# Kernel tuning notes

Hardware: AMD Instinct MI355X
Metric: run time of the kernel (lower is better)

## Reference

```python
import jax, jax.numpy as jnp
import numpy as np

E, N, D = 640000, 10000, 128  # edges, nodes, feature dim (edge=node=global=128)
H, O = 256, 128               # MLP hidden / output dims; concat dim = 4*D = 512


def setup_inputs() -> dict:
    key = jax.random.key(0)
    ks = jax.random.split(key, 7)
    return {
        "edge_attr": jax.random.normal(ks[0], (E, D), dtype=jnp.float32),
        "node_attr": jax.random.normal(ks[1], (N, D), dtype=jnp.float32),
        "global_attr": jax.random.normal(ks[2], (D,), dtype=jnp.float32),
        "senders": jax.random.randint(ks[3], (E,), 0, N),
        "receivers": jax.random.randint(ks[4], (E,), 0, N),
        "W1": jax.random.normal(ks[5], (4 * D, H), dtype=jnp.float32) / np.float32(np.sqrt(4 * D)),
        "b1": jnp.zeros((H,), dtype=jnp.float32),
        "W2": jax.random.normal(ks[6], (H, O), dtype=jnp.float32) / np.float32(np.sqrt(H)),
        "b2": jnp.zeros((O,), dtype=jnp.float32),
    }


def reference(edge_attr, node_attr, global_attr, senders, receivers, W1, b1, W2, b2):
    # Batched form of the per-edge Python loop:
    #   cat([e.data, e.receiver.data, e.sender.data, G.global_attribute.data]) -> updater MLP
    num_edges = edge_attr.shape[0]
    g = jnp.broadcast_to(global_attr, (num_edges, global_attr.shape[0]))  # [E, Dg]
    x = jnp.concatenate(
        [edge_attr, node_attr[receivers], node_attr[senders], g], axis=-1
    )  # [E, 4D]
    h = jax.nn.relu(x @ W1 + b1)  # [E, H]
    return h @ W2 + b2            # [E, O] : updated edge attributes
```

## Files before the change

### kernel.cpp

```cpp
#include <hip/hip_runtime.h>
#include <hip/hip_bf16.h>


typedef __attribute__((ext_vector_type(8))) short bf16x8;
typedef __attribute__((ext_vector_type(4))) float f32x4;
typedef __attribute__((ext_vector_type(2))) unsigned int u32x2;

static __device__ __forceinline__ unsigned short f2bf(float f) {
    unsigned u = __builtin_bit_cast(unsigned, f);
    u += 0x7FFFu + ((u >> 16) & 1u);
    return (unsigned short)(u >> 16);
}

static __device__ __forceinline__ unsigned cvt_pk_bf16(float lo, float hi) {
    unsigned r;
    asm("v_cvt_pk_bf16_f32 %0, %1, %2" : "=v"(r) : "v"(lo), "v"(hi));
    return r;
}


__global__ void prep_node_kernel(const float* __restrict__ node,
                                 ushort* __restrict__ nb) {
    int i = blockIdx.x * 256 + threadIdx.x;
    if (i >= 160000) return;
    const float4* s = (const float4*)(node + (size_t)i * 8);
    float4 a = s[0], b = s[1];
    ushort tmp[8] = { f2bf(a.x), f2bf(a.y), f2bf(a.z), f2bf(a.w),
                      f2bf(b.x), f2bf(b.y), f2bf(b.z), f2bf(b.w) };
    *(bf16x8*)&nb[(size_t)i * 8] = *(bf16x8*)tmp;
}

__global__ void prep_w1_kernel(const float* __restrict__ W1,
                               ushort* __restrict__ w1f) {
    int id = blockIdx.x * 256 + threadIdx.x;
    if (id >= 16 * 12 * 64) return;
    int l = id & 63, blk = id >> 6;
    int ks = blk % 12, gnt = blk / 12;
    int n  = gnt * 16 + (l & 15);
    int k0 = ks * 32 + (l >> 4) * 8;
    ushort tmp[8];
    #pragma unroll
    for (int j = 0; j < 8; ++j) tmp[j] = f2bf(W1[(k0 + j) * 256 + n]);
    *(bf16x8*)&w1f[(size_t)id * 8] = *(bf16x8*)tmp;
}

__global__ void prep_w2_kernel(const float* __restrict__ W2,
                               ushort* __restrict__ w2f) {
    int id = blockIdx.x * 256 + threadIdx.x;
    if (id >= 8 * 8 * 64) return;
    int l = id & 63, blk = id >> 6;
    int ks = blk % 8, gnt = blk / 8;
    int n  = gnt * 16 + (l & 15);
    int k0 = ks * 32 + (l >> 4) * 8;
    ushort tmp[8];
    #pragma unroll
    for (int j = 0; j < 8; ++j) tmp[j] = f2bf(W2[(k0 + j) * 128 + n]);
    *(bf16x8*)&w2f[(size_t)id * 8] = *(bf16x8*)tmp;
}

__global__ void prep_hbias_kernel(const float* __restrict__ W1,
                                  const float* __restrict__ b1,
                                  const float* __restrict__ g,
                                  float* __restrict__ hbias) {
    int n = threadIdx.x;
    float acc = b1[n];
    for (int k = 0; k < 128; ++k) acc += g[k] * W1[(384 + k) * 256 + n];
    hbias[n] = acc;
}


__global__ __launch_bounds__(256, 4) void edge_mlp_kernel(
    const float* __restrict__ edge_attr,
    const int* __restrict__ senders,
    const int* __restrict__ receivers,
    const ushort* __restrict__ node_bf,
    const ushort* __restrict__ w1f,
    const ushort* __restrict__ w2f,
    const float* __restrict__ hbias,
    const float* __restrict__ b2,
    float* __restrict__ out)
{
    __shared__ ushort Lds[64 * 256];
    ushort* Xe = Lds;
    ushort* Hs = Lds;

    const int t    = threadIdx.x;
    const int l    = t & 63;
    const int wid  = t >> 6;
    const int base = blockIdx.x * 64;

    const int lr = l & 15;
    const int q  = l >> 4;
    const int lk = q * 8;

    int nrow[4], srow[4];
    #pragma unroll
    for (int mt = 0; mt < 4; ++mt) {
        int e = base + mt * 16 + lr;
        nrow[mt] = receivers[e] * 128;
        srow[mt] = senders[e]   * 128;
    }

    #pragma unroll
    for (int p = 0; p < 4; ++p) {
        int chunk = p * 256 + t;
        int r  = chunk >> 4;
        int c0 = (chunk & 15) * 8;
        const float4* src = (const float4*)(edge_attr + (size_t)(base + r) * 128 + c0);
        float4 a = src[0];
        float4 b = src[1];
        uint4 uu = { cvt_pk_bf16(a.x, a.y), cvt_pk_bf16(a.z, a.w),
                     cvt_pk_bf16(b.x, b.y), cvt_pk_bf16(b.z, b.w) };
        *(bf16x8*)&Xe[r * 128 + (c0 ^ ((r & 7) << 3))] = __builtin_bit_cast(bf16x8, uu);
    }

    __syncthreads();

    f32x4 acc[4][4];
    #pragma unroll
    for (int mt = 0; mt < 4; ++mt)
        #pragma unroll
        for (int nt = 0; nt < 4; ++nt)
            acc[mt][nt] = (f32x4){0.f, 0.f, 0.f, 0.f};

    #pragma unroll
    for (int ks = 0; ks < 4; ++ks) {
        bf16x8 B[4];
        #pragma unroll
        for (int nt = 0; nt < 4; ++nt)
            B[nt] = *(const bf16x8*)&w1f[(size_t)(((wid * 4 + nt) * 12 + ks) * 64 + l) * 8];
        bf16x8 X[4];
        const int kk = ks * 32 + lk;
        #pragma unroll
        for (int mt = 0; mt < 4; ++mt) {
            const int row = mt * 16 + lr;
            X[mt] = *(const bf16x8*)&Xe[row * 128 + (kk ^ ((row & 7) << 3))];
        }
        #pragma unroll
        for (int mt = 0; mt < 4; ++mt)
            #pragma unroll
            for (int nt = 0; nt < 4; ++nt)
                acc[mt][nt] = __builtin_amdgcn_mfma_f32_16x16x32_bf16(
                    B[nt], X[mt], acc[mt][nt], 0, 0, 0);
    }

    __syncthreads();

    #pragma unroll
    for (int ks = 4; ks < 12; ++ks) {
        bf16x8 B[4];
        #pragma unroll
        for (int nt = 0; nt < 4; ++nt)
            B[nt] = *(const bf16x8*)&w1f[(size_t)(((wid * 4 + nt) * 12 + ks) * 64 + l) * 8];
        const int off = ((ks - 4) & 3) * 32 + lk;
        bf16x8 X[4];
        #pragma unroll
        for (int mt = 0; mt < 4; ++mt)
            X[mt] = *(const bf16x8*)&node_bf[(ks < 8 ? nrow[mt] : srow[mt]) + off];
        #pragma unroll
        for (int mt = 0; mt < 4; ++mt)
            #pragma unroll
            for (int nt = 0; nt < 4; ++nt)
                acc[mt][nt] = __builtin_amdgcn_mfma_f32_16x16x32_bf16(
                    B[nt], X[mt], acc[mt][nt], 0, 0, 0);
    }

    #pragma unroll
    for (int nt = 0; nt < 4; ++nt) {
        const int F = wid * 64 + nt * 16 + q * 4;
        float4 hb4 = *(const float4*)&hbias[F];
        #pragma unroll
        for (int mt = 0; mt < 4; ++mt) {
            float v0 = fmaxf(acc[mt][nt][0] + hb4.x, 0.f);
            float v1 = fmaxf(acc[mt][nt][1] + hb4.y, 0.f);
            float v2 = fmaxf(acc[mt][nt][2] + hb4.z, 0.f);
            float v3 = fmaxf(acc[mt][nt][3] + hb4.w, 0.f);
            u32x2 w = { cvt_pk_bf16(v0, v1), cvt_pk_bf16(v2, v3) };
            const int edge = mt * 16 + lr;
            *(u32x2*)&Hs[edge * 256 + (F ^ ((edge & 7) << 3))] = w;
        }
    }

    __syncthreads();

    f32x4 acc2[4][2];
    #pragma unroll
    for (int mt = 0; mt < 4; ++mt)
        #pragma unroll
        for (int nt = 0; nt < 2; ++nt)
            acc2[mt][nt] = (f32x4){0.f, 0.f, 0.f, 0.f};

    #pragma unroll
    for (int ks = 0; ks < 8; ++ks) {
        bf16x8 W[2];
        #pragma unroll
        for (int nt = 0; nt < 2; ++nt)
            W[nt] = *(const bf16x8*)&w2f[(size_t)(((wid * 2 + nt) * 8 + ks) * 64 + l) * 8];
        bf16x8 Hfr[4];
        const int F = ks * 32 + lk;
        #pragma unroll
        for (int mt = 0; mt < 4; ++mt) {
            const int edge = mt * 16 + lr;
            Hfr[mt] = *(const bf16x8*)&Hs[edge * 256 + (F ^ ((edge & 7) << 3))];
        }
        #pragma unroll
        for (int mt = 0; mt < 4; ++mt)
            #pragma unroll
            for (int nt = 0; nt < 2; ++nt)
                acc2[mt][nt] = __builtin_amdgcn_mfma_f32_16x16x32_bf16(
                    W[nt], Hfr[mt], acc2[mt][nt], 0, 0, 0);
    }

    #pragma unroll
    for (int nt = 0; nt < 2; ++nt) {
        const int F = wid * 32 + nt * 16 + q * 4;
        float4 b24 = *(const float4*)&b2[F];
        #pragma unroll
        for (int mt = 0; mt < 4; ++mt) {
            float4 o = { acc2[mt][nt][0] + b24.x, acc2[mt][nt][1] + b24.y,
                         acc2[mt][nt][2] + b24.z, acc2[mt][nt][3] + b24.w };
            *(float4*)&out[(size_t)(base + mt * 16 + lr) * 128 + F] = o;
        }
    }
}


extern "C" void kernel_launch(void* const* d_in, const int* in_sizes, int n_in,
                              void* d_out, int out_size, void* d_ws, size_t ws_size,
                              hipStream_t stream) {
    (void)in_sizes; (void)n_in; (void)out_size; (void)ws_size;

    const float* edge_attr   = (const float*)d_in[0];
    const float* node_attr   = (const float*)d_in[1];
    const float* global_attr = (const float*)d_in[2];
    const int*   senders     = (const int*)d_in[3];
    const int*   receivers   = (const int*)d_in[4];
    const float* W1          = (const float*)d_in[5];
    const float* b1          = (const float*)d_in[6];
    const float* W2          = (const float*)d_in[7];
    const float* b2          = (const float*)d_in[8];
    float* out = (float*)d_out;

    ushort* node_bf = (ushort*)d_ws;
    ushort* w1f     = (ushort*)((char*)d_ws + 2560000);
    ushort* w2f     = (ushort*)((char*)d_ws + 2756608);
    float*  hbias   = (float*)((char*)d_ws + 2822144);

    hipLaunchKernelGGL(prep_node_kernel,  dim3(625), dim3(256), 0, stream, node_attr, node_bf);
    hipLaunchKernelGGL(prep_w1_kernel,    dim3(48),  dim3(256), 0, stream, W1, w1f);
    hipLaunchKernelGGL(prep_w2_kernel,    dim3(16),  dim3(256), 0, stream, W2, w2f);
    hipLaunchKernelGGL(prep_hbias_kernel, dim3(1),   dim3(256), 0, stream, W1, b1, global_attr, hbias);

    hipLaunchKernelGGL(edge_mlp_kernel, dim3(10000), dim3(256), 0, stream,
                       edge_attr, senders, receivers, node_bf, w1f, w2f, hbias, b2, out);
}
```

Measured before the change: 377.6 us.

## Use 128-edge blocks with 8 waves and double-buffer weight fragment loads

Each block now has 512 threads and handles 128 edges, with two wave rows of 64 edges each sharing the same weight columns. The two layer-1 loops are merged into one 12-step loop. W1 and W2 fragments are prefetched one k-step ahead into double buffers so the global loads overlap the MFMAs. LDS doubles to 64KB per block and register pressure rises from the prefetch buffers, which may lower occupancy.

```diff
diff --git a/kernel.cpp b/kernel.cpp
--- a/kernel.cpp
+++ b/kernel.cpp
@@ -69,7 +69,7 @@
 }
 
 
-__global__ __launch_bounds__(256, 4) void edge_mlp_kernel(
+__global__ __launch_bounds__(512, 4) void edge_mlp_kernel(
     const float* __restrict__ edge_attr,
     const int* __restrict__ senders,
     const int* __restrict__ receivers,
@@ -80,14 +80,16 @@
     const float* __restrict__ b2,
     float* __restrict__ out)
 {
-    __shared__ ushort Lds[64 * 256];
+    __shared__ ushort Lds[128 * 256];
     ushort* Xe = Lds;
     ushort* Hs = Lds;
 
     const int t    = threadIdx.x;
     const int l    = t & 63;
     const int wid  = t >> 6;
-    const int base = blockIdx.x * 64;
+    const int wm   = wid >> 2;
+    const int wn   = wid & 3;
+    const int base = blockIdx.x * 128;
 
     const int lr = l & 15;
     const int q  = l >> 4;
@@ -96,14 +98,14 @@
     int nrow[4], srow[4];
     #pragma unroll
     for (int mt = 0; mt < 4; ++mt) {
-        int e = base + mt * 16 + lr;
+        int e = base + wm * 64 + mt * 16 + lr;
         nrow[mt] = receivers[e] * 128;
         srow[mt] = senders[e]   * 128;
     }
 
     #pragma unroll
     for (int p = 0; p < 4; ++p) {
-        int chunk = p * 256 + t;
+        int chunk = p * 512 + t;
         int r  = chunk >> 4;
         int c0 = (chunk & 15) * 8;
         const float4* src = (const float4*)(edge_attr + (size_t)(base + r) * 128 + c0);
@@ -123,51 +125,47 @@
         for (int nt = 0; nt < 4; ++nt)
             acc[mt][nt] = (f32x4){0.f, 0.f, 0.f, 0.f};
 
-    #pragma unroll
-    for (int ks = 0; ks < 4; ++ks) {
-        bf16x8 B[4];
-        #pragma unroll
-        for (int nt = 0; nt < 4; ++nt)
-            B[nt] = *(const bf16x8*)&w1f[(size_t)(((wid * 4 + nt) * 12 + ks) * 64 + l) * 8];
+    bf16x8 B[2][4];
+    #pragma unroll
+    for (int nt = 0; nt < 4; ++nt)
+        B[0][nt] = *(const bf16x8*)&w1f[(size_t)(((wn * 4 + nt) * 12 + 0) * 64 + l) * 8];
+
+    #pragma unroll
+    for (int ks = 0; ks < 12; ++ks) {
+        const int cur = ks & 1;
+        if (ks < 11) {
+            #pragma unroll
+            for (int nt = 0; nt < 4; ++nt)
+                B[cur ^ 1][nt] = *(const bf16x8*)&w1f[
+                    (size_t)(((wn * 4 + nt) * 12 + (ks + 1)) * 64 + l) * 8];
+        }
         bf16x8 X[4];
-        const int kk = ks * 32 + lk;
-        #pragma unroll
-        for (int mt = 0; mt < 4; ++mt) {
-            const int row = mt * 16 + lr;
-            X[mt] = *(const bf16x8*)&Xe[row * 128 + (kk ^ ((row & 7) << 3))];
+        if (ks < 4) {
+            const int kk = ks * 32 + lk;
+            #pragma unroll
+            for (int mt = 0; mt < 4; ++mt) {
+                const int row = wm * 64 + mt * 16 + lr;
+                X[mt] = *(const bf16x8*)&Xe[row * 128 + (kk ^ ((row & 7) << 3))];
+            }
+        } else {
+            const int off = (ks & 3) * 32 + lk;
+            #pragma unroll
+            for (int mt = 0; mt < 4; ++mt)
+                X[mt] = *(const bf16x8*)&node_bf[(ks < 8 ? nrow[mt] : srow[mt]) + off];
         }
         #pragma unroll
         for (int mt = 0; mt < 4; ++mt)
             #pragma unroll
             for (int nt = 0; nt < 4; ++nt)
                 acc[mt][nt] = __builtin_amdgcn_mfma_f32_16x16x32_bf16(
-                    B[nt], X[mt], acc[mt][nt], 0, 0, 0);
+                    B[cur][nt], X[mt], acc[mt][nt], 0, 0, 0);
     }
 
     __syncthreads();
 
     #pragma unroll
-    for (int ks = 4; ks < 12; ++ks) {
-        bf16x8 B[4];
-        #pragma unroll
-        for (int nt = 0; nt < 4; ++nt)
-            B[nt] = *(const bf16x8*)&w1f[(size_t)(((wid * 4 + nt) * 12 + ks) * 64 + l) * 8];
-        const int off = ((ks - 4) & 3) * 32 + lk;
-        bf16x8 X[4];
-        #pragma unroll
-        for (int mt = 0; mt < 4; ++mt)
-            X[mt] = *(const bf16x8*)&node_bf[(ks < 8 ? nrow[mt] : srow[mt]) + off];
-        #pragma unroll
-        for (int mt = 0; mt < 4; ++mt)
-            #pragma unroll
-            for (int nt = 0; nt < 4; ++nt)
-                acc[mt][nt] = __builtin_amdgcn_mfma_f32_16x16x32_bf16(
-                    B[nt], X[mt], acc[mt][nt], 0, 0, 0);
-    }
-
-    #pragma unroll
     for (int nt = 0; nt < 4; ++nt) {
-        const int F = wid * 64 + nt * 16 + q * 4;
+        const int F = wn * 64 + nt * 16 + q * 4;
         float4 hb4 = *(const float4*)&hbias[F];
         #pragma unroll
         for (int mt = 0; mt < 4; ++mt) {
@@ -176,7 +174,7 @@
             float v2 = fmaxf(acc[mt][nt][2] + hb4.z, 0.f);
             float v3 = fmaxf(acc[mt][nt][3] + hb4.w, 0.f);
             u32x2 w = { cvt_pk_bf16(v0, v1), cvt_pk_bf16(v2, v3) };
-            const int edge = mt * 16 + lr;
+            const int edge = wm * 64 + mt * 16 + lr;
             *(u32x2*)&Hs[edge * 256 + (F ^ ((edge & 7) << 3))] = w;
         }
     }
@@ -190,17 +188,25 @@
         for (int nt = 0; nt < 2; ++nt)
             acc2[mt][nt] = (f32x4){0.f, 0.f, 0.f, 0.f};
 
+    bf16x8 W2b[2][2];
+    #pragma unroll
+    for (int nt = 0; nt < 2; ++nt)
+        W2b[0][nt] = *(const bf16x8*)&w2f[(size_t)(((wn * 2 + nt) * 8 + 0) * 64 + l) * 8];
+
     #pragma unroll
     for (int ks = 0; ks < 8; ++ks) {
-        bf16x8 W[2];
-        #pragma unroll
-        for (int nt = 0; nt < 2; ++nt)
-            W[nt] = *(const bf16x8*)&w2f[(size_t)(((wid * 2 + nt) * 8 + ks) * 64 + l) * 8];
+        const int cur = ks & 1;
+        if (ks < 7) {
+            #pragma unroll
+            for (int nt = 0; nt < 2; ++nt)
+                W2b[cur ^ 1][nt] = *(const bf16x8*)&w2f[
+                    (size_t)(((wn * 2 + nt) * 8 + (ks + 1)) * 64 + l) * 8];
+        }
         bf16x8 Hfr[4];
         const int F = ks * 32 + lk;
         #pragma unroll
         for (int mt = 0; mt < 4; ++mt) {
-            const int edge = mt * 16 + lr;
+            const int edge = wm * 64 + mt * 16 + lr;
             Hfr[mt] = *(const bf16x8*)&Hs[edge * 256 + (F ^ ((edge & 7) << 3))];
         }
         #pragma unroll
@@ -208,18 +214,18 @@
             #pragma unroll
             for (int nt = 0; nt < 2; ++nt)
                 acc2[mt][nt] = __builtin_amdgcn_mfma_f32_16x16x32_bf16(
-                    W[nt], Hfr[mt], acc2[mt][nt], 0, 0, 0);
+                    W2b[cur][nt], Hfr[mt], acc2[mt][nt], 0, 0, 0);
     }
 
     #pragma unroll
     for (int nt = 0; nt < 2; ++nt) {
-        const int F = wid * 32 + nt * 16 + q * 4;
+        const int F = wn * 32 + nt * 16 + q * 4;
         float4 b24 = *(const float4*)&b2[F];
         #pragma unroll
         for (int mt = 0; mt < 4; ++mt) {
             float4 o = { acc2[mt][nt][0] + b24.x, acc2[mt][nt][1] + b24.y,
                          acc2[mt][nt][2] + b24.z, acc2[mt][nt][3] + b24.w };
-            *(float4*)&out[(size_t)(base + mt * 16 + lr) * 128 + F] = o;
+            *(float4*)&out[(size_t)(base + wm * 64 + mt * 16 + lr) * 128 + F] = o;
         }
     }
 }
@@ -251,6 +257,6 @@
     hipLaunchKernelGGL(prep_w2_kernel,    dim3(16),  dim3(256), 0, stream, W2, w2f);
     hipLaunchKernelGGL(prep_hbias_kernel, dim3(1),   dim3(256), 0, stream, W1, b1, global_attr, hbias);
 
-    hipLaunchKernelGGL(edge_mlp_kernel, dim3(10000), dim3(256), 0, stream,
+    hipLaunchKernelGGL(edge_mlp_kernel, dim3(5000), dim3(512), 0, stream,
                        edge_attr, senders, receivers, node_bf, w1f, w2f, hbias, b2, out);
 }
```

New measurement: 427.2 us. +13.2%, slower.

## Precompute per-node W1 projections and gather them instead of node features

Applied to the files above, without the earlier changes.

Splits the first layer algebraically: each node's receiver and sender contributions (node_attr @ W1 slices, plus the global bias folded into the receiver part) are computed once per node in a new prep kernel and stored as bf16. The edge kernel then only runs the edge-feature K=128 GEMM and adds the two gathered 256-wide projections before ReLU. This cuts the layer-1 MFMA work per edge by two thirds, but gathers twice as many bytes per node and adds an extra bf16 rounding of the projections. It also double-buffers the weight fragment loads, separates the Xe and Hs LDS buffers, and lowers the occupancy hint from 4 to 3.

```diff
diff --git a/kernel.cpp b/kernel.cpp
--- a/kernel.cpp
+++ b/kernel.cpp
@@ -18,17 +18,13 @@
     return r;
 }
 
-
-__global__ void prep_node_kernel(const float* __restrict__ node,
-                                 ushort* __restrict__ nb) {
-    int i = blockIdx.x * 256 + threadIdx.x;
-    if (i >= 160000) return;
-    const float4* s = (const float4*)(node + (size_t)i * 8);
-    float4 a = s[0], b = s[1];
-    ushort tmp[8] = { f2bf(a.x), f2bf(a.y), f2bf(a.z), f2bf(a.w),
-                      f2bf(b.x), f2bf(b.y), f2bf(b.z), f2bf(b.w) };
-    *(bf16x8*)&nb[(size_t)i * 8] = *(bf16x8*)tmp;
-}
+static __device__ __forceinline__ float bflo(unsigned u) {
+    return __builtin_bit_cast(float, u << 16);
+}
+static __device__ __forceinline__ float bfhi(unsigned u) {
+    return __builtin_bit_cast(float, u & 0xFFFF0000u);
+}
+
 
 __global__ void prep_w1_kernel(const float* __restrict__ W1,
                                ushort* __restrict__ w1f) {
@@ -68,21 +64,100 @@
     hbias[n] = acc;
 }
 
-
-__global__ __launch_bounds__(256, 4) void edge_mlp_kernel(
+__global__ __launch_bounds__(256) void prep_proj_kernel(
+    const float* __restrict__ node_attr,
+    const ushort* __restrict__ w1f,
+    const float* __restrict__ hbias,
+    ushort* __restrict__ Pr,
+    ushort* __restrict__ Ps)
+{
+    __shared__ ushort Xn[64 * 128];
+
+    const int t = threadIdx.x, l = t & 63, wn = t >> 6;
+    const int base = blockIdx.x * 64;
+    const int lr = l & 15, q = l >> 4, lk = q * 8;
+
+    #pragma unroll
+    for (int p = 0; p < 4; ++p) {
+        int chunk = p * 256 + t;
+        int r  = chunk >> 4;
+        int c0 = (chunk & 15) * 8;
+        int node = base + r; if (node >= 10000) node = 9999;
+        const float4* src = (const float4*)(node_attr + (size_t)node * 128 + c0);
+        float4 a = src[0];
+        float4 b = src[1];
+        uint4 uu = { cvt_pk_bf16(a.x, a.y), cvt_pk_bf16(a.z, a.w),
+                     cvt_pk_bf16(b.x, b.y), cvt_pk_bf16(b.z, b.w) };
+        *(bf16x8*)&Xn[r * 128 + (c0 ^ ((r & 7) << 3))] = __builtin_bit_cast(bf16x8, uu);
+    }
+    __syncthreads();
+
+    #pragma unroll
+    for (int s = 0; s < 2; ++s) {
+        f32x4 acc[4][4];
+        #pragma unroll
+        for (int mt = 0; mt < 4; ++mt)
+            #pragma unroll
+            for (int nt = 0; nt < 4; ++nt)
+                acc[mt][nt] = (f32x4){0.f, 0.f, 0.f, 0.f};
+
+        #pragma unroll
+        for (int ks = 0; ks < 4; ++ks) {
+            bf16x8 B[4];
+            #pragma unroll
+            for (int nt = 0; nt < 4; ++nt)
+                B[nt] = *(const bf16x8*)&w1f[
+                    (size_t)(((wn * 4 + nt) * 12 + 4 + s * 4 + ks) * 64 + l) * 8];
+            bf16x8 X[4];
+            const int kk = ks * 32 + lk;
+            #pragma unroll
+            for (int mt = 0; mt < 4; ++mt) {
+                const int row = mt * 16 + lr;
+                X[mt] = *(const bf16x8*)&Xn[row * 128 + (kk ^ ((row & 7) << 3))];
+            }
+            #pragma unroll
+            for (int mt = 0; mt < 4; ++mt)
+                #pragma unroll
+                for (int nt = 0; nt < 4; ++nt)
+                    acc[mt][nt] = __builtin_amdgcn_mfma_f32_16x16x32_bf16(
+                        B[nt], X[mt], acc[mt][nt], 0, 0, 0);
+        }
+
+        ushort* P = s ? Ps : Pr;
+        #pragma unroll
+        for (int nt = 0; nt < 4; ++nt) {
+            const int F = wn * 64 + nt * 16 + q * 4;
+            float4 hb4 = {0.f, 0.f, 0.f, 0.f};
+            if (s == 0) hb4 = *(const float4*)&hbias[F];
+            #pragma unroll
+            for (int mt = 0; mt < 4; ++mt) {
+                const int node = base + mt * 16 + lr;
+                if (node < 10000) {
+                    u32x2 w = { cvt_pk_bf16(acc[mt][nt][0] + hb4.x,
+                                            acc[mt][nt][1] + hb4.y),
+                                cvt_pk_bf16(acc[mt][nt][2] + hb4.z,
+                                            acc[mt][nt][3] + hb4.w) };
+                    *(u32x2*)&P[(size_t)node * 256 + F] = w;
+                }
+            }
+        }
+    }
+}
+
+
+__global__ __launch_bounds__(256, 3) void edge_mlp_kernel(
     const float* __restrict__ edge_attr,
     const int* __restrict__ senders,
     const int* __restrict__ receivers,
-    const ushort* __restrict__ node_bf,
     const ushort* __restrict__ w1f,
     const ushort* __restrict__ w2f,
-    const float* __restrict__ hbias,
+    const ushort* __restrict__ Pr,
+    const ushort* __restrict__ Ps,
     const float* __restrict__ b2,
     float* __restrict__ out)
 {
-    __shared__ ushort Lds[64 * 256];
-    ushort* Xe = Lds;
-    ushort* Hs = Lds;
+    __shared__ ushort Xe[64 * 128];
+    __shared__ ushort Hs[64 * 256];
 
     const int t    = threadIdx.x;
     const int l    = t & 63;
@@ -93,12 +168,12 @@
     const int q  = l >> 4;
     const int lk = q * 8;
 
-    int nrow[4], srow[4];
+    int pr_off[4], ps_off[4];
     #pragma unroll
     for (int mt = 0; mt < 4; ++mt) {
         int e = base + mt * 16 + lr;
-        nrow[mt] = receivers[e] * 128;
-        srow[mt] = senders[e]   * 128;
+        pr_off[mt] = receivers[e] * 256;
+        ps_off[mt] = senders[e]   * 256;
     }
 
     #pragma unroll
@@ -123,12 +198,20 @@
         for (int nt = 0; nt < 4; ++nt)
             acc[mt][nt] = (f32x4){0.f, 0.f, 0.f, 0.f};
 
+    bf16x8 B[2][4];
+    #pragma unroll
+    for (int nt = 0; nt < 4; ++nt)
+        B[0][nt] = *(const bf16x8*)&w1f[(size_t)(((wid * 4 + nt) * 12 + 0) * 64 + l) * 8];
+
     #pragma unroll
     for (int ks = 0; ks < 4; ++ks) {
-        bf16x8 B[4];
-        #pragma unroll
-        for (int nt = 0; nt < 4; ++nt)
-            B[nt] = *(const bf16x8*)&w1f[(size_t)(((wid * 4 + nt) * 12 + ks) * 64 + l) * 8];
+        const int cur = ks & 1;
+        if (ks < 3) {
+            #pragma unroll
+            for (int nt = 0; nt < 4; ++nt)
+                B[cur ^ 1][nt] = *(const bf16x8*)&w1f[
+                    (size_t)(((wid * 4 + nt) * 12 + (ks + 1)) * 64 + l) * 8];
+        }
         bf16x8 X[4];
         const int kk = ks * 32 + lk;
         #pragma unroll
@@ -141,40 +224,30 @@
             #pragma unroll
             for (int nt = 0; nt < 4; ++nt)
                 acc[mt][nt] = __builtin_amdgcn_mfma_f32_16x16x32_bf16(
-                    B[nt], X[mt], acc[mt][nt], 0, 0, 0);
-    }
-
-    __syncthreads();
-
-    #pragma unroll
-    for (int ks = 4; ks < 12; ++ks) {
-        bf16x8 B[4];
-        #pragma unroll
-        for (int nt = 0; nt < 4; ++nt)
-            B[nt] = *(const bf16x8*)&w1f[(size_t)(((wid * 4 + nt) * 12 + ks) * 64 + l) * 8];
-        const int off = ((ks - 4) & 3) * 32 + lk;
-        bf16x8 X[4];
-        #pragma unroll
-        for (int mt = 0; mt < 4; ++mt)
-            X[mt] = *(const bf16x8*)&node_bf[(ks < 8 ? nrow[mt] : srow[mt]) + off];
-        #pragma unroll
-        for (int mt = 0; mt < 4; ++mt)
-            #pragma unroll
-            for (int nt = 0; nt < 4; ++nt)
-                acc[mt][nt] = __builtin_amdgcn_mfma_f32_16x16x32_bf16(
-                    B[nt], X[mt], acc[mt][nt], 0, 0, 0);
-    }
-
+                    B[cur][nt], X[mt], acc[mt][nt], 0, 0, 0);
+    }
+
+    u32x2 pg[4][4], sg[4][4];
     #pragma unroll
     for (int nt = 0; nt < 4; ++nt) {
         const int F = wid * 64 + nt * 16 + q * 4;
-        float4 hb4 = *(const float4*)&hbias[F];
-        #pragma unroll
-        for (int mt = 0; mt < 4; ++mt) {
-            float v0 = fmaxf(acc[mt][nt][0] + hb4.x, 0.f);
-            float v1 = fmaxf(acc[mt][nt][1] + hb4.y, 0.f);
-            float v2 = fmaxf(acc[mt][nt][2] + hb4.z, 0.f);
-            float v3 = fmaxf(acc[mt][nt][3] + hb4.w, 0.f);
+        #pragma unroll
+        for (int mt = 0; mt < 4; ++mt) {
+            pg[nt][mt] = *(const u32x2*)&Pr[pr_off[mt] + F];
+            sg[nt][mt] = *(const u32x2*)&Ps[ps_off[mt] + F];
+        }
+    }
+
+    #pragma unroll
+    for (int nt = 0; nt < 4; ++nt) {
+        const int F = wid * 64 + nt * 16 + q * 4;
+        #pragma unroll
+        for (int mt = 0; mt < 4; ++mt) {
+            u32x2 p = pg[nt][mt], s = sg[nt][mt];
+            float v0 = fmaxf(acc[mt][nt][0] + bflo(p.x) + bflo(s.x), 0.f);
+            float v1 = fmaxf(acc[mt][nt][1] + bfhi(p.x) + bfhi(s.x), 0.f);
+            float v2 = fmaxf(acc[mt][nt][2] + bflo(p.y) + bflo(s.y), 0.f);
+            float v3 = fmaxf(acc[mt][nt][3] + bfhi(p.y) + bfhi(s.y), 0.f);
             u32x2 w = { cvt_pk_bf16(v0, v1), cvt_pk_bf16(v2, v3) };
             const int edge = mt * 16 + lr;
             *(u32x2*)&Hs[edge * 256 + (F ^ ((edge & 7) << 3))] = w;
@@ -190,12 +263,20 @@
         for (int nt = 0; nt < 2; ++nt)
             acc2[mt][nt] = (f32x4){0.f, 0.f, 0.f, 0.f};
 
+    bf16x8 W2b[2][2];
+    #pragma unroll
+    for (int nt = 0; nt < 2; ++nt)
+        W2b[0][nt] = *(const bf16x8*)&w2f[(size_t)(((wid * 2 + nt) * 8 + 0) * 64 + l) * 8];
+
     #pragma unroll
     for (int ks = 0; ks < 8; ++ks) {
-        bf16x8 W[2];
-        #pragma unroll
-        for (int nt = 0; nt < 2; ++nt)
-            W[nt] = *(const bf16x8*)&w2f[(size_t)(((wid * 2 + nt) * 8 + ks) * 64 + l) * 8];
+        const int cur = ks & 1;
+        if (ks < 7) {
+            #pragma unroll
+            for (int nt = 0; nt < 2; ++nt)
+                W2b[cur ^ 1][nt] = *(const bf16x8*)&w2f[
+                    (size_t)(((wid * 2 + nt) * 8 + (ks + 1)) * 64 + l) * 8];
+        }
         bf16x8 Hfr[4];
         const int F = ks * 32 + lk;
         #pragma unroll
@@ -208,7 +289,7 @@
             #pragma unroll
             for (int nt = 0; nt < 2; ++nt)
                 acc2[mt][nt] = __builtin_amdgcn_mfma_f32_16x16x32_bf16(
-                    W[nt], Hfr[mt], acc2[mt][nt], 0, 0, 0);
+                    W2b[cur][nt], Hfr[mt], acc2[mt][nt], 0, 0, 0);
     }
 
     #pragma unroll
@@ -241,16 +322,18 @@
     const float* b2          = (const float*)d_in[8];
     float* out = (float*)d_out;
 
-    ushort* node_bf = (ushort*)d_ws;
-    ushort* w1f     = (ushort*)((char*)d_ws + 2560000);
-    ushort* w2f     = (ushort*)((char*)d_ws + 2756608);
-    float*  hbias   = (float*)((char*)d_ws + 2822144);
-
-    hipLaunchKernelGGL(prep_node_kernel,  dim3(625), dim3(256), 0, stream, node_attr, node_bf);
+    ushort* w1f   = (ushort*)d_ws;
+    ushort* w2f   = (ushort*)((char*)d_ws + 196608);
+    float*  hbias = (float*)((char*)d_ws + 262144);
+    ushort* Pr    = (ushort*)((char*)d_ws + 263168);
+    ushort* Ps    = (ushort*)((char*)d_ws + 5383168);
+
     hipLaunchKernelGGL(prep_w1_kernel,    dim3(48),  dim3(256), 0, stream, W1, w1f);
     hipLaunchKernelGGL(prep_w2_kernel,    dim3(16),  dim3(256), 0, stream, W2, w2f);
     hipLaunchKernelGGL(prep_hbias_kernel, dim3(1),   dim3(256), 0, stream, W1, b1, global_attr, hbias);
+    hipLaunchKernelGGL(prep_proj_kernel,  dim3(157), dim3(256), 0, stream,
+                       node_attr, w1f, hbias, Pr, Ps);
 
     hipLaunchKernelGGL(edge_mlp_kernel, dim3(10000), dim3(256), 0, stream,
-                       edge_attr, senders, receivers, node_bf, w1f, w2f, hbias, b2, out);
-}
+                       edge_attr, senders, receivers, w1f, w2f, Pr, Ps, b2, out);
+}
```

Measured after the change: 312.6 us. -17.2%, faster.
